# Kernel tuning notes

Measured on AMD Instinct MI355X. Metric: run time of the kernel, lower is better.

The kernel has to match this reference:

```python
import jax, jax.numpy as jnp
import numpy as np

B, D_IN, H = 128, 256, 256


def setup_inputs() -> dict:
    key = jax.random.key(0)
    ks = jax.random.split(key, 16)
    d = {}
    d["x_t"] = jax.random.normal(ks[0], (B, D_IN), jnp.float32)
    d["h_c1"] = jax.random.normal(ks[1], (B, H), jnp.float32)
    d["h_c2"] = jax.random.normal(ks[2], (B, H), jnp.float32)
    for i in range(4):
        d[f"gm{i}"] = jax.random.normal(ks[3 + i], (B, H), jnp.float32) * 0.1
    for i in range(4, 8):
        d[f"gm{i}"] = jax.random.normal(ks[3 + i], (B, D_IN, H), jnp.float32) * 0.1
    # exp-exp parameterization: r = exp(-exp(r_param)) with r ~ U(0,1)
    u_r = jax.random.uniform(ks[11], (1, H), jnp.float32, 0.01, 0.99)
    d["r_param"] = jnp.log(-jnp.log(u_r))
    # theta = exp(theta_param) with theta ~ U(0, pi)
    u_t = jax.random.uniform(ks[12], (1, H), jnp.float32, 0.01, float(np.pi))
    d["theta_param"] = jnp.log(u_t)
    scale = 1.0 / np.sqrt(D_IN)
    d["wx1"] = jax.random.normal(ks[13], (D_IN, H), jnp.float32) * scale
    d["wx2"] = jax.random.normal(ks[14], (D_IN, H), jnp.float32) * scale
    return d


def reference(x_t, h_c1, h_c2, gm0, gm1, gm2, gm3, gm4, gm5, gm6, gm7,
              r_param, theta_param, wx1, wx2):
    h_c1 = jax.lax.stop_gradient(h_c1)
    h_c2 = jax.lax.stop_gradient(h_c2)

    # exp-exp parameterization of the complex pole g + i*phi
    exp_r = jnp.exp(r_param)          # (1, H)
    r = jnp.exp(-exp_r)               # |pole| in (0, 1)
    theta = jnp.exp(theta_param)      # pole angle
    g = r * jnp.cos(theta)
    phi = r * jnp.sin(theta)
    norm = jnp.sqrt(1.0 - r * r)      # input normalization

    w1x = x_t @ wx1                   # (B, H)
    w2x = x_t @ wx2

    c1 = g * h_c1 - phi * h_c2 + norm * w1x
    c2 = g * h_c2 + phi * h_c1 + norm * w2x

    h1_post = jax.nn.relu(c1)
    h2_post = jax.nn.relu(c2)
    d1 = (c1 > 0).astype(c1.dtype)
    d2 = (c2 > 0).astype(c2.dtype)

    # derivatives of (g, phi, norm) wrt r_param / theta_param
    d_g_w_r = -exp_r * g
    d_phi_w_r = -exp_r * phi
    d_g_w_th = -theta * phi
    d_phi_w_th = theta * g
    d_norm_w_r = exp_r * (r * r) / norm

    # eligibility traces for r_param / theta_param: (B, H)
    ngm0 = d1 * (d_g_w_r * h_c1 + g * gm0 - d_phi_w_r * h_c2 - phi * gm1 + d_norm_w_r * w1x)
    ngm1 = d2 * (d_g_w_r * h_c2 + g * gm1 + d_phi_w_r * h_c1 + phi * gm0 + d_norm_w_r * w2x)
    ngm2 = d1 * (d_g_w_th * h_c1 + g * gm2 - d_phi_w_th * h_c2 - phi * gm3)
    ngm3 = d2 * (d_g_w_th * h_c2 + g * gm3 + d_phi_w_th * h_c1 + phi * gm2)

    # eligibility traces for input weights: (B, D_in, H); outer product x_t ⊗ norm
    x_outer = x_t[:, :, None]         # (B, D, 1) broadcasts against (1, H)
    d1e = d1[:, None, :]
    d2e = d2[:, None, :]
    ngm4 = d1e * (g * gm4 - phi * gm5 + norm * x_outer)  # c1 wrt wx1
    ngm5 = d2e * (g * gm5 + phi * gm4)                   # c2 wrt wx1
    ngm6 = d1e * (g * gm6 - phi * gm7)                   # c1 wrt wx2
    ngm7 = d2e * (g * gm7 + phi * gm6 + norm * x_outer)  # c2 wrt wx2

    new_gm = tuple(jax.lax.stop_gradient(t) for t in (ngm0, ngm1, ngm2, ngm3, ngm4, ngm5, ngm6, ngm7))
    return (h1_post, h2_post) + new_gm
```

## Files before the change

kernel.cpp:

```cpp
#include <hip/hip_runtime.h>

#define B    128
#define D_IN 256
#define H    256

#define BH      (B * H)
#define BIG     (B * D_IN * H)
#define OFF_H1   0
#define OFF_H2   (1 * BH)
#define OFF_NGM0 (2 * BH)
#define OFF_NGM1 (3 * BH)
#define OFF_NGM2 (4 * BH)
#define OFF_NGM3 (5 * BH)
#define OFF_NGM4 (6 * BH)
#define OFF_NGM5 (OFF_NGM4 + 1 * BIG)
#define OFF_NGM6 (OFF_NGM4 + 2 * BIG)
#define OFF_NGM7 (OFF_NGM4 + 3 * BIG)

__global__ __launch_bounds__(H) void k_small(
    const float* __restrict__ x,   const float* __restrict__ hc1, const float* __restrict__ hc2,
    const float* __restrict__ gm0, const float* __restrict__ gm1,
    const float* __restrict__ gm2, const float* __restrict__ gm3,
    const float* __restrict__ rp,  const float* __restrict__ thp,
    const float* __restrict__ wx1, const float* __restrict__ wx2,
    float* __restrict__ out, float* __restrict__ ws)
{
    const int b = blockIdx.x;
    const int h = threadIdx.x;

    __shared__ float xs[D_IN];
    xs[h] = x[b * D_IN + h];
    __syncthreads();

    const float er  = expf(rp[h]);
    const float r   = expf(-er);
    const float th  = expf(thp[h]);
    const float g   = r * cosf(th);
    const float phi = r * sinf(th);
    const float nrm = sqrtf(1.0f - r * r);

    float acc1 = 0.0f, acc2 = 0.0f;
#pragma unroll 8
    for (int k = 0; k < D_IN; ++k) {
        const float xv = xs[k];
        acc1 = fmaf(xv, wx1[k * H + h], acc1);
        acc2 = fmaf(xv, wx2[k * H + h], acc2);
    }

    const int idx = b * H + h;
    const float h1 = hc1[idx], h2 = hc2[idx];

    const float c1 = g * h1 - phi * h2 + nrm * acc1;
    const float c2 = g * h2 + phi * h1 + nrm * acc2;
    const float d1 = (c1 > 0.0f) ? 1.0f : 0.0f;
    const float d2 = (c2 > 0.0f) ? 1.0f : 0.0f;

    out[OFF_H1 + idx] = fmaxf(c1, 0.0f);
    out[OFF_H2 + idx] = fmaxf(c2, 0.0f);

    const float m0 = gm0[idx], m1 = gm1[idx], m2 = gm2[idx], m3 = gm3[idx];

    const float dgr = -er * g;
    const float dpr = -er * phi;
    const float dgt = -th * phi;
    const float dpt =  th * g;
    const float dnr =  er * r * r / nrm;

    out[OFF_NGM0 + idx] = d1 * (dgr * h1 + g * m0 - dpr * h2 - phi * m1 + dnr * acc1);
    out[OFF_NGM1 + idx] = d2 * (dgr * h2 + g * m1 + dpr * h1 + phi * m0 + dnr * acc2);
    out[OFF_NGM2 + idx] = d1 * (dgt * h1 + g * m2 - dpt * h2 - phi * m3);
    out[OFF_NGM3 + idx] = d2 * (dgt * h2 + g * m3 + dpt * h1 + phi * m2);

    ws[0 * BH + idx] = d1 * g;
    ws[1 * BH + idx] = d1 * phi;
    ws[2 * BH + idx] = d1 * nrm;
    ws[3 * BH + idx] = d2 * g;
    ws[4 * BH + idx] = d2 * phi;
    ws[5 * BH + idx] = d2 * nrm;
}

__global__ __launch_bounds__(256) void k_big(
    const float4* __restrict__ gm4, const float4* __restrict__ gm5,
    const float4* __restrict__ gm6, const float4* __restrict__ gm7,
    const float*  __restrict__ x,
    const float4* __restrict__ wsq,
    float4* __restrict__ o4, float4* __restrict__ o5,
    float4* __restrict__ o6, float4* __restrict__ o7)
{
    const int t  = blockIdx.x * 256 + threadIdx.x;
    const int b  = t >> 12;
    const int jg = (t >> 6) & 63;
    const int h4 = t & 63;

    const int CQ = BH / 4;
    const int ci = (b << 6) + h4;

    const float4 A1 = wsq[0 * CQ + ci];
    const float4 B1 = wsq[1 * CQ + ci];
    const float4 N1 = wsq[2 * CQ + ci];
    const float4 A2 = wsq[3 * CQ + ci];
    const float4 B2 = wsq[4 * CQ + ci];
    const float4 N2 = wsq[5 * CQ + ci];

    const int base_j = jg << 2;

#pragma unroll
    for (int jj = 0; jj < 4; ++jj) {
        const int j = base_j + jj;
        const int i = (b << 14) + (j << 6) + h4;

        const float xv = x[(b << 8) + j];

        const float4 g4 = gm4[i], g5 = gm5[i], g6 = gm6[i], g7 = gm7[i];

        float4 r4, r5, r6, r7;
#define COMP(c)                                                       \
        r4.c = fmaf(N1.c, xv, fmaf(A1.c, g4.c, -(B1.c * g5.c)));      \
        r5.c = fmaf(A2.c, g5.c, B2.c * g4.c);                         \
        r6.c = fmaf(A1.c, g6.c, -(B1.c * g7.c));                      \
        r7.c = fmaf(N2.c, xv, fmaf(A2.c, g7.c, B2.c * g6.c));
        COMP(x) COMP(y) COMP(z) COMP(w)
#undef COMP

        o4[i] = r4;
        o5[i] = r5;
        o6[i] = r6;
        o7[i] = r7;
    }
}

extern "C" void kernel_launch(void* const* d_in, const int* in_sizes, int n_in,
                              void* d_out, int out_size, void* d_ws, size_t ws_size,
                              hipStream_t stream) {
    const float* x_t  = (const float*)d_in[0];
    const float* hc1  = (const float*)d_in[1];
    const float* hc2  = (const float*)d_in[2];
    const float* gm0  = (const float*)d_in[3];
    const float* gm1  = (const float*)d_in[4];
    const float* gm2  = (const float*)d_in[5];
    const float* gm3  = (const float*)d_in[6];
    const float* gm4  = (const float*)d_in[7];
    const float* gm5  = (const float*)d_in[8];
    const float* gm6  = (const float*)d_in[9];
    const float* gm7  = (const float*)d_in[10];
    const float* rp   = (const float*)d_in[11];
    const float* thp  = (const float*)d_in[12];
    const float* wx1  = (const float*)d_in[13];
    const float* wx2  = (const float*)d_in[14];

    float* out = (float*)d_out;
    float* ws  = (float*)d_ws;

    k_small<<<B, H, 0, stream>>>(x_t, hc1, hc2, gm0, gm1, gm2, gm3,
                                 rp, thp, wx1, wx2, out, ws);

    const int threads_total = B * 64 * 64;
    k_big<<<threads_total / 256, 256, 0, stream>>>(
        (const float4*)gm4, (const float4*)gm5, (const float4*)gm6, (const float4*)gm7,
        x_t, (const float4*)ws,
        (float4*)(out + OFF_NGM4), (float4*)(out + OFF_NGM5),
        (float4*)(out + OFF_NGM6), (float4*)(out + OFF_NGM7));
}
```

Baseline: 285.5 us.

## Split-K vectorized matvec in small kernel and one-quad-per-thread big kernel

The small kernel's x@W matvec now has each thread load float4 weight columns over a quarter of the K range, then reduces the four partial sums through shared memory. Each thread does fewer serial iterations and issues wider loads. The big elementwise kernel drops its four-iteration loop so each thread handles one float4 per tensor, with four times as many blocks. This raises parallelism and memory-level concurrency but reloads the six coefficient float4s once per quad instead of once per four quads.

New measurement: 311.1 us. 9.0% more time.

```diff
diff --git a/kernel.cpp b/kernel.cpp
--- a/kernel.cpp
+++ b/kernel.cpp
@@ -17,7 +17,7 @@
 #define OFF_NGM6 (OFF_NGM4 + 2 * BIG)
 #define OFF_NGM7 (OFF_NGM4 + 3 * BIG)
 
-__global__ __launch_bounds__(H) void k_small(
+__global__ __launch_bounds__(256) void k_small(
     const float* __restrict__ x,   const float* __restrict__ hc1, const float* __restrict__ hc2,
     const float* __restrict__ gm0, const float* __restrict__ gm1,
     const float* __restrict__ gm2, const float* __restrict__ gm3,
@@ -26,11 +26,46 @@
     float* __restrict__ out, float* __restrict__ ws)
 {
     const int b = blockIdx.x;
-    const int h = threadIdx.x;
+    const int t = threadIdx.x;
 
-    __shared__ float xs[D_IN];
-    xs[h] = x[b * D_IN + h];
+    __shared__ float  xs[D_IN];
+    __shared__ float4 s1q[4 * 64];
+    __shared__ float4 s2q[4 * 64];
+
+    xs[t] = x[b * D_IN + t];
     __syncthreads();
+
+    const int hq = t & 63;
+    const int ks = t >> 6;
+
+    const float4* __restrict__ wx1q = (const float4*)wx1;
+    const float4* __restrict__ wx2q = (const float4*)wx2;
+
+    float4 a1 = make_float4(0.f, 0.f, 0.f, 0.f);
+    float4 a2 = make_float4(0.f, 0.f, 0.f, 0.f);
+    const int k0 = ks * 64;
+#pragma unroll 8
+    for (int kk = 0; kk < 64; ++kk) {
+        const int k = k0 + kk;
+        const float xv = xs[k];
+        const float4 w1 = wx1q[k * 64 + hq];
+        const float4 w2 = wx2q[k * 64 + hq];
+        a1.x = fmaf(xv, w1.x, a1.x); a1.y = fmaf(xv, w1.y, a1.y);
+        a1.z = fmaf(xv, w1.z, a1.z); a1.w = fmaf(xv, w1.w, a1.w);
+        a2.x = fmaf(xv, w2.x, a2.x); a2.y = fmaf(xv, w2.y, a2.y);
+        a2.z = fmaf(xv, w2.z, a2.z); a2.w = fmaf(xv, w2.w, a2.w);
+    }
+    s1q[ks * 64 + hq] = a1;
+    s2q[ks * 64 + hq] = a2;
+    __syncthreads();
+
+    const int h = t;
+    const float* s1f = (const float*)s1q;
+    const float* s2f = (const float*)s2q;
+    const float acc1 = s1f[0 * 256 + h] + s1f[1 * 256 + h]
+                     + s1f[2 * 256 + h] + s1f[3 * 256 + h];
+    const float acc2 = s2f[0 * 256 + h] + s2f[1 * 256 + h]
+                     + s2f[2 * 256 + h] + s2f[3 * 256 + h];
 
     const float er  = expf(rp[h]);
     const float r   = expf(-er);
@@ -38,14 +73,6 @@
     const float g   = r * cosf(th);
     const float phi = r * sinf(th);
     const float nrm = sqrtf(1.0f - r * r);
-
-    float acc1 = 0.0f, acc2 = 0.0f;
-#pragma unroll 8
-    for (int k = 0; k < D_IN; ++k) {
-        const float xv = xs[k];
-        acc1 = fmaf(xv, wx1[k * H + h], acc1);
-        acc2 = fmaf(xv, wx2[k * H + h], acc2);
-    }
 
     const int idx = b * H + h;
     const float h1 = hc1[idx], h2 = hc2[idx];
@@ -87,10 +114,10 @@
     float4* __restrict__ o4, float4* __restrict__ o5,
     float4* __restrict__ o6, float4* __restrict__ o7)
 {
-    const int t  = blockIdx.x * 256 + threadIdx.x;
-    const int b  = t >> 12;
-    const int jg = (t >> 6) & 63;
-    const int h4 = t & 63;
+    const int i  = blockIdx.x * 256 + threadIdx.x;
+    const int b  = i >> 14;
+    const int j  = (i >> 6) & (D_IN - 1);
+    const int h4 = i & 63;
 
     const int CQ = BH / 4;
     const int ci = (b << 6) + h4;
@@ -102,31 +129,23 @@
     const float4 B2 = wsq[4 * CQ + ci];
     const float4 N2 = wsq[5 * CQ + ci];
 
-    const int base_j = jg << 2;
+    const float xv = x[(b << 8) + j];
 
-#pragma unroll
-    for (int jj = 0; jj < 4; ++jj) {
-        const int j = base_j + jj;
-        const int i = (b << 14) + (j << 6) + h4;
+    const float4 g4 = gm4[i], g5 = gm5[i], g6 = gm6[i], g7 = gm7[i];
 
-        const float xv = x[(b << 8) + j];
-
-        const float4 g4 = gm4[i], g5 = gm5[i], g6 = gm6[i], g7 = gm7[i];
-
-        float4 r4, r5, r6, r7;
+    float4 r4, r5, r6, r7;
 #define COMP(c)                                                       \
-        r4.c = fmaf(N1.c, xv, fmaf(A1.c, g4.c, -(B1.c * g5.c)));      \
-        r5.c = fmaf(A2.c, g5.c, B2.c * g4.c);                         \
-        r6.c = fmaf(A1.c, g6.c, -(B1.c * g7.c));                      \
-        r7.c = fmaf(N2.c, xv, fmaf(A2.c, g7.c, B2.c * g6.c));
-        COMP(x) COMP(y) COMP(z) COMP(w)
+    r4.c = fmaf(N1.c, xv, fmaf(A1.c, g4.c, -(B1.c * g5.c)));          \
+    r5.c = fmaf(A2.c, g5.c, B2.c * g4.c);                             \
+    r6.c = fmaf(A1.c, g6.c, -(B1.c * g7.c));                          \
+    r7.c = fmaf(N2.c, xv, fmaf(A2.c, g7.c, B2.c * g6.c));
+    COMP(x) COMP(y) COMP(z) COMP(w)
 #undef COMP
 
-        o4[i] = r4;
-        o5[i] = r5;
-        o6[i] = r6;
-        o7[i] = r7;
-    }
+    o4[i] = r4;
+    o5[i] = r5;
+    o6[i] = r6;
+    o7[i] = r7;
 }
 
 extern "C" void kernel_launch(void* const* d_in, const int* in_sizes, int n_in,
@@ -151,11 +170,11 @@
     float* out = (float*)d_out;
     float* ws  = (float*)d_ws;
 
-    k_small<<<B, H, 0, stream>>>(x_t, hc1, hc2, gm0, gm1, gm2, gm3,
-                                 rp, thp, wx1, wx2, out, ws);
+    k_small<<<B, 256, 0, stream>>>(x_t, hc1, hc2, gm0, gm1, gm2, gm3,
+                                   rp, thp, wx1, wx2, out, ws);
 
-    const int threads_total = B * 64 * 64;
-    k_big<<<threads_total / 256, 256, 0, stream>>>(
+    const int quads = BIG / 4;
+    k_big<<<quads / 256, 256, 0, stream>>>(
         (const float4*)gm4, (const float4*)gm5, (const float4*)gm6, (const float4*)gm7,
         x_t, (const float4*)ws,
         (float4*)(out + OFF_NGM4), (float4*)(out + OFF_NGM5),
```
